# Kernel tuning notes

Hardware: AMD Instinct MI355X
Metric: run time of the kernel (lower is better)

Reference implementation:

```python
import jax, jax.numpy as jnp
import numpy as np

K = 8          # number of nearest neighbors (init kwarg k)
CONST = 0.1    # inverseweight const
NUM = 1.0      # inverseweight num


def setup_inputs() -> dict:
    key = jax.random.key(0)
    k1, k2 = jax.random.split(key)
    data1 = jax.random.normal(k1, (4096, 1024), dtype=jnp.float32)
    data2 = jax.random.normal(k2, (8192, 1024), dtype=jnp.float32)
    return {"data1": data1, "data2": data2}


def reference(data1, data2):
    # pairwise Euclidean distance (torch.dist with p=2): [N, M]
    x2 = jnp.sum(data1 * data1, axis=1, keepdims=True)          # [N, 1]
    y2 = jnp.sum(data2 * data2, axis=1)                         # [M]
    d2 = x2 + y2[None, :] - 2.0 * (data1 @ data2.T)             # [N, M]
    dist = jnp.sqrt(jnp.maximum(d2, 1e-12))

    # k smallest distances and their indices
    neg_top, idx = jax.lax.top_k(-dist, K)                      # [N, K]
    knn_dist = -neg_top                                         # [N, K]

    # inverse weighting: w = num / (dist + const)
    w = NUM / (knn_dist + CONST)                                # [N, K]

    # gather neighbor vectors and weighted-average them
    neigh = data2[idx]                                          # [N, K, D]
    out = jnp.einsum('nk,nkd->nd', w, neigh) / jnp.sum(w, axis=1, keepdims=True)
    return out
```

## Files before the change

### kernel.cpp

```cpp
#include <hip/hip_runtime.h>


typedef short bf16x8 __attribute__((ext_vector_type(8)));
typedef float f32x4 __attribute__((ext_vector_type(4)));

#define SENTINEL 1e30f
#define BKK 32

static __device__ __forceinline__ unsigned short f2bf(float f) {
  unsigned u = __float_as_uint(f);
  return (unsigned short)((u + 0x7fffu + ((u >> 16) & 1u)) >> 16);
}

__global__ __launch_bounds__(256) void convert_all_kernel(
    const float* __restrict__ A, const float* __restrict__ B,
    unsigned short* __restrict__ Abf, unsigned short* __restrict__ Bbf,
    float* __restrict__ y2, int N) {
  const int bid = blockIdx.x;
  const int tid = threadIdx.x;
  if (bid < N) {
    const float4 v = ((const float4*)&A[(size_t)bid * 1024])[tid];
    ushort4 o;
    o.x = f2bf(v.x); o.y = f2bf(v.y); o.z = f2bf(v.z); o.w = f2bf(v.w);
    ((ushort4*)&Abf[(size_t)bid * 1024])[tid] = o;
  } else {
    const int m = bid - N;
    __shared__ float red[256];
    const float4 v = ((const float4*)&B[(size_t)m * 1024])[tid];
    ushort4 o;
    o.x = f2bf(v.x); o.y = f2bf(v.y); o.z = f2bf(v.z); o.w = f2bf(v.w);
    ((ushort4*)&Bbf[(size_t)m * 1024])[tid] = o;
    red[tid] = v.x * v.x + v.y * v.y + v.z * v.z + v.w * v.w;
    __syncthreads();
    for (int s = 128; s > 0; s >>= 1) {
      if (tid < s) red[tid] += red[tid + s];
      __syncthreads();
    }
    if (tid == 0) y2[m] = red[0];
  }
}

#define CAS(sa, ia, sb, ib)                         \
  do {                                              \
    if ((sa) > (sb)) {                              \
      const float _t = (sa); (sa) = (sb); (sb) = _t;\
      const int _u = (ia); (ia) = (ib); (ib) = _u;  \
    }                                               \
  } while (0)

#define STAGE(sk, b)                                                          \
  do {                                                                        \
    const unsigned short* gA_ =                                               \
        Abf + (size_t)(r0 + w * 32 + srow) * 1024 + (sk) * 32 + sofs;         \
    const unsigned short* gB_ =                                               \
        Bbf + (size_t)(c0 + w * 64 + srow) * 1024 + (sk) * 32 + sofs;         \
    __builtin_amdgcn_global_load_lds(                                         \
        (const __attribute__((address_space(1))) void*)gA_,                   \
        (__attribute__((address_space(3))) void*)&As[b][(w * 32) * 32],       \
        16, 0, 0);                                                            \
    __builtin_amdgcn_global_load_lds(                                         \
        (const __attribute__((address_space(1))) void*)(gA_ + (size_t)16 * 1024), \
        (__attribute__((address_space(3))) void*)&As[b][(w * 32 + 16) * 32],  \
        16, 0, 0);                                                            \
    _Pragma("unroll")                                                         \
    for (int l_ = 0; l_ < 4; ++l_)                                            \
      __builtin_amdgcn_global_load_lds(                                       \
          (const __attribute__((address_space(1))) void*)(gB_ + (size_t)(16 * l_) * 1024), \
          (__attribute__((address_space(3))) void*)&Bs[b][(w * 64 + 16 * l_) * 32], \
          16, 0, 0);                                                          \
  } while (0)

#define COMPUTE(b)                                                            \
  do {                                                                        \
    bf16x8 af[4], bfr[8];                                                     \
    _Pragma("unroll")                                                         \
    for (int fi = 0; fi < 4; ++fi)                                            \
      af[fi] = *(const bf16x8*)&As[b][(frowA + fi * 16) * 32 + fofs];         \
    _Pragma("unroll")                                                         \
    for (int fj = 0; fj < 8; ++fj)                                            \
      bfr[fj] = *(const bf16x8*)&Bs[b][(frowB + fj * 16) * 32 + fofs];        \
    _Pragma("unroll")                                                         \
    for (int fi = 0; fi < 4; ++fi)                                            \
      _Pragma("unroll")                                                       \
      for (int fj = 0; fj < 8; ++fj)                                          \
        acc[fi][fj] = __builtin_amdgcn_mfma_f32_16x16x32_bf16(                \
            bfr[fj], af[fi], acc[fi][fj], 0, 0, 0);                           \
  } while (0)

__global__ __launch_bounds__(256, 2) void screen5_kernel(
    const unsigned short* __restrict__ Abf, const unsigned short* __restrict__ Bbf,
    const float* __restrict__ y2g,
    float* __restrict__ cand_s, int* __restrict__ cand_i) {
  __shared__ unsigned short As[2][128 * 32];
  __shared__ unsigned short Bs[2][256 * 32];
  __shared__ float y2sh[256];

  const int tid = threadIdx.x;
  const int w = tid >> 6;
  const int lane = tid & 63;
  const int wr = w >> 1, wc = w & 1;

  const int v = blockIdx.x + gridDim.x * blockIdx.y;
  const int bx = (v & 7) * 2 + ((v >> 3) & 1);
  const int by = v >> 4;
  const int r0 = by * 128;

  const int srow = lane >> 2;
  const int sofs = ((lane & 3) ^ ((lane >> 3) & 3)) * 8;

  const int frowA = wr * 64 + (lane & 15);
  const int frowB = wc * 128 + (lane & 15);
  const int fofs = ((lane >> 4) ^ ((lane >> 1) & 3)) * 8;
  const int cgrp = (lane >> 4) * 4;

  for (int chunk = 0; chunk < 2; ++chunk) {
    const int c0 = bx * 512 + chunk * 256;
    __syncthreads();
    y2sh[tid] = y2g[c0 + tid];

    f32x4 acc[4][8];
#pragma unroll
    for (int fi = 0; fi < 4; ++fi)
#pragma unroll
      for (int fj = 0; fj < 8; ++fj) {
        f32x4 z = {0.f, 0.f, 0.f, 0.f};
        acc[fi][fj] = z;
      }

    STAGE(0, 0);
    for (int kk = 0; kk < 32; kk += 2) {
      __syncthreads();
      STAGE(kk + 1, 1);
      COMPUTE(0);
      __syncthreads();
      if (kk + 2 < 32) STAGE(kk + 2, 0);
      COMPUTE(1);
    }

    float4 y2v[8];
#pragma unroll
    for (int fj = 0; fj < 8; ++fj)
      y2v[fj] = *(const float4*)&y2sh[wc * 128 + fj * 16 + cgrp];

#pragma unroll
    for (int fi = 0; fi < 4; ++fi) {
      float ls[8];
      int li[8];
#pragma unroll
      for (int j = 0; j < 8; ++j) { ls[j] = SENTINEL; li[j] = 0x7fffffff; }
      const int cb = c0 + wc * 128 + cgrp;
#pragma unroll
      for (int fj = 0; fj < 8; ++fj) {
#pragma unroll
        for (int reg = 0; reg < 4; ++reg) {
          const float s = y2v[fj][reg] - 2.0f * acc[fi][fj][reg];
          if (s < ls[7]) {
            ls[7] = s; li[7] = cb + fj * 16 + reg;
#pragma unroll
            for (int j = 7; j > 0; --j) {
              if (ls[j] < ls[j - 1]) {
                const float t = ls[j]; ls[j] = ls[j - 1]; ls[j - 1] = t;
                const int u = li[j]; li[j] = li[j - 1]; li[j - 1] = u;
              }
            }
          }
        }
      }
#pragma unroll
      for (int off = 16; off <= 32; off <<= 1) {
        float rs[8];
        int ri[8];
#pragma unroll
        for (int j = 0; j < 8; ++j) {
          rs[j] = __shfl_xor(ls[j], off, 64);
          ri[j] = __shfl_xor(li[j], off, 64);
        }
        float ms[8];
        int mi_[8];
#pragma unroll
        for (int i = 0; i < 8; ++i) {
          const bool t = ls[i] < rs[7 - i];
          ms[i] = t ? ls[i] : rs[7 - i];
          mi_[i] = t ? li[i] : ri[7 - i];
        }
        CAS(ms[0], mi_[0], ms[4], mi_[4]);
        CAS(ms[1], mi_[1], ms[5], mi_[5]);
        CAS(ms[2], mi_[2], ms[6], mi_[6]);
        CAS(ms[3], mi_[3], ms[7], mi_[7]);
        CAS(ms[0], mi_[0], ms[2], mi_[2]);
        CAS(ms[1], mi_[1], ms[3], mi_[3]);
        CAS(ms[4], mi_[4], ms[6], mi_[6]);
        CAS(ms[5], mi_[5], ms[7], mi_[7]);
        CAS(ms[0], mi_[0], ms[1], mi_[1]);
        CAS(ms[2], mi_[2], ms[3], mi_[3]);
        CAS(ms[4], mi_[4], ms[5], mi_[5]);
        CAS(ms[6], mi_[6], ms[7], mi_[7]);
#pragma unroll
        for (int j = 0; j < 8; ++j) { ls[j] = ms[j]; li[j] = mi_[j]; }
      }
      if ((lane >> 4) == 0) {
        const int row = r0 + wr * 64 + fi * 16 + lane;
        const size_t base =
            ((size_t)row * 64 + wc * 32 + bx * 2 + chunk) * 8;
#pragma unroll
        for (int j = 0; j < 8; ++j) {
          cand_s[base + j] = ls[j];
          cand_i[base + j] = li[j];
        }
      }
    }
  }
}

__global__ __launch_bounds__(256) void finalize4_kernel(
    const float* __restrict__ A, const float* __restrict__ B,
    const float* __restrict__ y2g,
    const float* __restrict__ cand_s, const int* __restrict__ cand_i,
    float* __restrict__ out) {
  const int tid = threadIdx.x;
  const int w = tid >> 6;
  const int lane = tid & 63;
  const int rloc = w >> 1;
  const int wh = w & 1;
  const int n = blockIdx.x * 2 + rloc;
  __shared__ int mi[2][512];
  __shared__ float comb[2][2][16];

  unsigned long long key[8];
#pragma unroll
  for (int i = 0; i < 8; ++i) {
    const int slot = lane + 64 * i;
    const float s = cand_s[(size_t)n * 512 + slot];
    if (wh == 0) mi[rloc][slot] = cand_i[(size_t)n * 512 + slot];
    unsigned u = __float_as_uint(s);
    u = (u & 0x80000000u) ? ~u : (u | 0x80000000u);
    key[i] = ((unsigned long long)u << 32) | (unsigned)slot;
  }
  __syncthreads();

  int ci[12];
  for (int r = 0; r < 12; ++r) {
    unsigned long long kb = key[0];
#pragma unroll
    for (int i = 1; i < 8; ++i) kb = key[i] < kb ? key[i] : kb;
#pragma unroll
    for (int off = 32; off >= 1; off >>= 1) {
      const unsigned long long o = __shfl_xor(kb, off, 64);
      kb = o < kb ? o : kb;
    }
    const int slot = (int)(kb & 0xffffffffu);
    ci[r] = mi[rloc][slot];
#pragma unroll
    for (int i = 0; i < 8; ++i)
      if (slot == lane + 64 * i) key[i] = ~0ull;
  }

  const float4* Arow = (const float4*)&A[(size_t)n * 1024];
  const int fbase = wh * 128 + lane * 2;
  float4 a4[2];
  a4[0] = Arow[fbase];
  a4[1] = Arow[fbase + 1];
  float part[13];
#pragma unroll
  for (int r = 0; r < 13; ++r) part[r] = 0.0f;
  part[12] = a4[0].x * a4[0].x + a4[0].y * a4[0].y + a4[0].z * a4[0].z +
             a4[0].w * a4[0].w + a4[1].x * a4[1].x + a4[1].y * a4[1].y +
             a4[1].z * a4[1].z + a4[1].w * a4[1].w;
#pragma unroll
  for (int p = 0; p < 2; ++p) {
    float4 b[12];
#pragma unroll
    for (int j = 0; j < 12; ++j)
      b[j] = ((const float4*)&B[(size_t)ci[j] * 1024])[fbase + p];
#pragma unroll
    for (int j = 0; j < 12; ++j)
      part[j] += a4[p].x * b[j].x + a4[p].y * b[j].y + a4[p].z * b[j].z +
                 a4[p].w * b[j].w;
  }
#pragma unroll
  for (int r = 0; r < 13; ++r) {
#pragma unroll
    for (int off = 32; off >= 1; off >>= 1) part[r] += __shfl_xor(part[r], off, 64);
  }
  if (lane == 0) {
#pragma unroll
    for (int r = 0; r < 13; ++r) comb[rloc][wh][r] = part[r];
  }
  __syncthreads();
  float tot[13];
#pragma unroll
  for (int r = 0; r < 13; ++r) tot[r] = comb[rloc][0][r] + comb[rloc][1][r];

  const float x2 = tot[12];
  float d2v[12];
  bool used[12];
#pragma unroll
  for (int j = 0; j < 12; ++j) {
    d2v[j] = x2 + y2g[ci[j]] - 2.0f * tot[j];
    used[j] = false;
  }
  float wk[8];
  int wi[8];
  float wsum = 0.0f;
  for (int k = 0; k < 8; ++k) {
    float bd = SENTINEL;
    int bi = 0x7fffffff, bslot = 0;
#pragma unroll
    for (int j = 0; j < 12; ++j) {
      if (used[j]) continue;
      const float d2 = d2v[j];
      if (d2 < bd || (d2 == bd && ci[j] < bi)) { bd = d2; bi = ci[j]; bslot = j; }
    }
    used[bslot] = true;
    const float d2c = fmaxf(bd, 1e-12f);
    const float wv = 1.0f / (sqrtf(d2c) + 0.1f);
    wk[k] = wv; wi[k] = bi; wsum += wv;
  }
  const float inv = 1.0f / wsum;

  float4 o0 = {0, 0, 0, 0}, o1 = {0, 0, 0, 0};
#pragma unroll
  for (int k = 0; k < 8; ++k) {
    const float wv = wk[k];
    const float4* Brow = (const float4*)&B[(size_t)wi[k] * 1024];
    const float4 b0 = Brow[fbase];
    const float4 b1 = Brow[fbase + 1];
    o0.x += wv * b0.x; o0.y += wv * b0.y; o0.z += wv * b0.z; o0.w += wv * b0.w;
    o1.x += wv * b1.x; o1.y += wv * b1.y; o1.z += wv * b1.z; o1.w += wv * b1.w;
  }
  o0.x *= inv; o0.y *= inv; o0.z *= inv; o0.w *= inv;
  o1.x *= inv; o1.y *= inv; o1.z *= inv; o1.w *= inv;
  float4* Orow = (float4*)&out[(size_t)n * 1024];
  Orow[fbase] = o0;
  Orow[fbase + 1] = o1;
}

__global__ __launch_bounds__(256) void rownorm_kernel(
    const float* __restrict__ B, float* __restrict__ y2) {
  const int m = blockIdx.x;
  const int tid = threadIdx.x;
  __shared__ float red[256];
  const float4 v = *(const float4*)&B[(size_t)m * 1024 + tid * 4];
  red[tid] = v.x * v.x + v.y * v.y + v.z * v.z + v.w * v.w;
  __syncthreads();
  for (int s = 128; s > 0; s >>= 1) {
    if (tid < s) red[tid] += red[tid + s];
    __syncthreads();
  }
  if (tid == 0) y2[m] = red[0];
}

__global__ __launch_bounds__(256) void knn_chunk_kernel(
    const float* __restrict__ A, const float* __restrict__ B,
    const float* __restrict__ y2g,
    float* __restrict__ cand_s, int* __restrict__ cand_i) {
  __shared__ float As[BKK][68];
  __shared__ float Bs[BKK][68];
  __shared__ float Sc[64][65];

  const int tid = threadIdx.x;
  const int tx = tid & 15;
  const int ty = tid >> 4;
  const int r0 = blockIdx.y * 64;
  const int c0 = blockIdx.x * 1024;
  const int lrow = tid >> 3;
  const int lk = (tid & 7) * 4;

  float top_s[8];
  int top_i[8];
#pragma unroll
  for (int j = 0; j < 8; ++j) { top_s[j] = SENTINEL; top_i[j] = 0x7fffffff; }

  for (int tile = 0; tile < 16; ++tile) {
    const int cbase = c0 + tile * 64;
    float acc[4][4];
#pragma unroll
    for (int i = 0; i < 4; ++i)
#pragma unroll
      for (int j = 0; j < 4; ++j) acc[i][j] = 0.0f;

    for (int k0 = 0; k0 < 1024; k0 += BKK) {
      const float4 a0 = *(const float4*)&A[(size_t)(r0 + lrow) * 1024 + k0 + lk];
      const float4 a1 = *(const float4*)&A[(size_t)(r0 + lrow + 32) * 1024 + k0 + lk];
      const float4 b0 = *(const float4*)&B[(size_t)(cbase + lrow) * 1024 + k0 + lk];
      const float4 b1 = *(const float4*)&B[(size_t)(cbase + lrow + 32) * 1024 + k0 + lk];
      __syncthreads();
      As[lk + 0][lrow] = a0.x; As[lk + 1][lrow] = a0.y;
      As[lk + 2][lrow] = a0.z; As[lk + 3][lrow] = a0.w;
      As[lk + 0][lrow + 32] = a1.x; As[lk + 1][lrow + 32] = a1.y;
      As[lk + 2][lrow + 32] = a1.z; As[lk + 3][lrow + 32] = a1.w;
      Bs[lk + 0][lrow] = b0.x; Bs[lk + 1][lrow] = b0.y;
      Bs[lk + 2][lrow] = b0.z; Bs[lk + 3][lrow] = b0.w;
      Bs[lk + 0][lrow + 32] = b1.x; Bs[lk + 1][lrow + 32] = b1.y;
      Bs[lk + 2][lrow + 32] = b1.z; Bs[lk + 3][lrow + 32] = b1.w;
      __syncthreads();
#pragma unroll
      for (int kk = 0; kk < BKK; ++kk) {
        const float4 av = *(const float4*)&As[kk][ty * 4];
        const float4 bv = *(const float4*)&Bs[kk][tx * 4];
        acc[0][0] += av.x * bv.x; acc[0][1] += av.x * bv.y;
        acc[0][2] += av.x * bv.z; acc[0][3] += av.x * bv.w;
        acc[1][0] += av.y * bv.x; acc[1][1] += av.y * bv.y;
        acc[1][2] += av.y * bv.z; acc[1][3] += av.y * bv.w;
        acc[2][0] += av.z * bv.x; acc[2][1] += av.z * bv.y;
        acc[2][2] += av.z * bv.z; acc[2][3] += av.z * bv.w;
        acc[3][0] += av.w * bv.x; acc[3][1] += av.w * bv.y;
        acc[3][2] += av.w * bv.z; acc[3][3] += av.w * bv.w;
      }
    }
#pragma unroll
    for (int i = 0; i < 4; ++i) {
      const int row = ty * 4 + i;
#pragma unroll
      for (int j = 0; j < 4; ++j) {
        const int col = tx * 4 + j;
        Sc[row][col] = y2g[cbase + col] - 2.0f * acc[i][j];
      }
    }
    __syncthreads();
    if (tid < 64) {
      for (int c = 0; c < 64; ++c) {
        const float s = Sc[tid][c];
        if (s < top_s[7]) {
          top_s[7] = s; top_i[7] = cbase + c;
#pragma unroll
          for (int j = 7; j > 0; --j) {
            if (top_s[j] < top_s[j - 1]) {
              const float tss = top_s[j]; top_s[j] = top_s[j - 1]; top_s[j - 1] = tss;
              const int tii = top_i[j]; top_i[j] = top_i[j - 1]; top_i[j - 1] = tii;
            }
          }
        }
      }
    }
  }

  if (tid < 64) {
    const int n = r0 + tid;
    const int base = (n * gridDim.x + blockIdx.x) * 8;
#pragma unroll
    for (int j = 0; j < 8; ++j) {
      cand_s[base + j] = top_s[j];
      cand_i[base + j] = top_i[j];
    }
  }
}

__global__ __launch_bounds__(256) void finalize_kernel(
    const float* __restrict__ A, const float* __restrict__ B,
    const float* __restrict__ cand_s, const int* __restrict__ cand_i,
    float* __restrict__ out, int nchunks) {
  const int n = blockIdx.x;
  const int tid = threadIdx.x;
  __shared__ float red[256];
  __shared__ float ls[64];
  __shared__ int li[64];
  __shared__ float wsh2[8];
  __shared__ int wid[8];
  __shared__ float wsum_sh;

  const int ncand = nchunks * 8;
  const float4 a = *(const float4*)&A[(size_t)n * 1024 + tid * 4];
  red[tid] = a.x * a.x + a.y * a.y + a.z * a.z + a.w * a.w;
  if (tid < ncand) {
    ls[tid] = cand_s[n * ncand + tid];
    li[tid] = cand_i[n * ncand + tid];
  }
  __syncthreads();
  for (int s = 128; s > 0; s >>= 1) {
    if (tid < s) red[tid] += red[tid + s];
    __syncthreads();
  }
  if (tid == 0) {
    const float x2 = red[0];
    float wsum = 0.0f;
    for (int j = 0; j < 8; ++j) {
      float bs = SENTINEL;
      int bi = 0x7fffffff;
      int bp = 0;
      for (int c = 0; c < ncand; ++c) {
        const float s_ = ls[c];
        const int i_ = li[c];
        if (s_ < bs || (s_ == bs && i_ < bi)) { bs = s_; bi = i_; bp = c; }
      }
      ls[bp] = SENTINEL; li[bp] = 0x7fffffff;
      float d2 = x2 + bs;
      d2 = fmaxf(d2, 1e-12f);
      const float wkk = 1.0f / (sqrtf(d2) + 0.1f);
      wsh2[j] = wkk; wid[j] = bi;
      wsum += wkk;
    }
    wsum_sh = wsum;
  }
  __syncthreads();
  const float inv = 1.0f / wsum_sh;
  float ox = 0.0f, oy = 0.0f, oz = 0.0f, ow = 0.0f;
#pragma unroll
  for (int j = 0; j < 8; ++j) {
    const float wkk = wsh2[j];
    const float4 v = *(const float4*)&B[(size_t)wid[j] * 1024 + tid * 4];
    ox += wkk * v.x; oy += wkk * v.y; oz += wkk * v.z; ow += wkk * v.w;
  }
  float4 o;
  o.x = ox * inv; o.y = oy * inv; o.z = oz * inv; o.w = ow * inv;
  *(float4*)&out[(size_t)n * 1024 + tid * 4] = o;
}

extern "C" void kernel_launch(void* const* d_in, const int* in_sizes, int n_in,
                              void* d_out, int out_size, void* d_ws, size_t ws_size,
                              hipStream_t stream) {
  const float* A = (const float*)d_in[0];
  const float* Bm = (const float*)d_in[1];
  const int D = 1024;
  const int N = in_sizes[0] / D;
  const int M = in_sizes[1] / D;

  const size_t needA = (size_t)N * D * 2;
  const size_t needB = (size_t)M * D * 2;
  const size_t needC = (size_t)N * 512 * 4;
  const size_t need = needA + needB + (size_t)M * 4 + 2 * needC;

  if (ws_size >= need && M == 8192 && N % 128 == 0 && N % 2 == 0) {
    unsigned short* Abf = (unsigned short*)d_ws;
    unsigned short* Bbf = Abf + (size_t)N * D;
    float* y2 = (float*)(Bbf + (size_t)M * D);
    float* cand_s = y2 + M;
    int* cand_i = (int*)(cand_s + (size_t)N * 512);

    convert_all_kernel<<<N + M, 256, 0, stream>>>(A, Bm, Abf, Bbf, y2, N);
    dim3 g(M / 512, N / 128);
    screen5_kernel<<<g, 256, 0, stream>>>(Abf, Bbf, y2, cand_s, cand_i);
    finalize4_kernel<<<N / 2, 256, 0, stream>>>(A, Bm, y2, cand_s, cand_i,
                                                (float*)d_out);
  } else {
    float* y2 = (float*)d_ws;
    float* cand_s = y2 + M;
    int* cand_i = (int*)(cand_s + (size_t)N * 64);
    rownorm_kernel<<<M, 256, 0, stream>>>(Bm, y2);
    dim3 gridB(M / 1024, N / 64);
    knn_chunk_kernel<<<gridB, 256, 0, stream>>>(A, Bm, y2, cand_s, cand_i);
    finalize_kernel<<<N, 256, 0, stream>>>(A, Bm, cand_s, cand_i, (float*)d_out, M / 1024);
  }
}
```

Measured before the change: 339.6 us.

## Triple-buffer GEMM staging with vmcnt sync and bitonic-merge finalize candidate selection

The screening GEMM moves from double to triple buffering of the LDS tiles. It uses explicit vmcnt waits with a single barrier per k-step and raises wave priority around the MFMA block, so global-to-LDS loads can run two stages ahead of compute. The y2 shared-memory staging is dropped in favour of direct global reads after the loop. The finalize kernel replaces its 12-round wave-wide argmin extraction with a register-level xor-shuffle bitonic merge of per-lane sorted top-8 lists into a top-12, which removes the LDS index table and the serial reductions. Triple buffering raises LDS use per block, which may reduce occupancy. Tie-breaking among equal scores may also differ from before.

```diff
diff --git a/kernel.cpp b/kernel.cpp
--- a/kernel.cpp
+++ b/kernel.cpp
@@ -79,21 +79,30 @@
     _Pragma("unroll")                                                         \
     for (int fj = 0; fj < 8; ++fj)                                            \
       bfr[fj] = *(const bf16x8*)&Bs[b][(frowB + fj * 16) * 32 + fofs];        \
+    __builtin_amdgcn_s_setprio(1);                                            \
     _Pragma("unroll")                                                         \
     for (int fi = 0; fi < 4; ++fi)                                            \
       _Pragma("unroll")                                                       \
       for (int fj = 0; fj < 8; ++fj)                                          \
         acc[fi][fj] = __builtin_amdgcn_mfma_f32_16x16x32_bf16(                \
             bfr[fj], af[fi], acc[fi][fj], 0, 0, 0);                           \
+    __builtin_amdgcn_s_setprio(0);                                            \
   } while (0)
 
-__global__ __launch_bounds__(256, 2) void screen5_kernel(
+#define PIPE_SYNC(N)                                                          \
+  do {                                                                        \
+    asm volatile("s_waitcnt vmcnt(" #N ")" ::: "memory");                     \
+    __builtin_amdgcn_sched_barrier(0);                                        \
+    __builtin_amdgcn_s_barrier();                                             \
+    __builtin_amdgcn_sched_barrier(0);                                        \
+  } while (0)
+
+__global__ __launch_bounds__(256, 2) void screen6_kernel(
     const unsigned short* __restrict__ Abf, const unsigned short* __restrict__ Bbf,
     const float* __restrict__ y2g,
     float* __restrict__ cand_s, int* __restrict__ cand_i) {
-  __shared__ unsigned short As[2][128 * 32];
-  __shared__ unsigned short Bs[2][256 * 32];
-  __shared__ float y2sh[256];
+  __shared__ unsigned short As[3][128 * 32];
+  __shared__ unsigned short Bs[3][256 * 32];
 
   const int tid = threadIdx.x;
   const int w = tid >> 6;
@@ -116,7 +125,6 @@
   for (int chunk = 0; chunk < 2; ++chunk) {
     const int c0 = bx * 512 + chunk * 256;
     __syncthreads();
-    y2sh[tid] = y2g[c0 + tid];
 
     f32x4 acc[4][8];
 #pragma unroll
@@ -128,19 +136,22 @@
       }
 
     STAGE(0, 0);
-    for (int kk = 0; kk < 32; kk += 2) {
-      __syncthreads();
-      STAGE(kk + 1, 1);
-      COMPUTE(0);
-      __syncthreads();
-      if (kk + 2 < 32) STAGE(kk + 2, 0);
-      COMPUTE(1);
-    }
+    STAGE(1, 1);
+    int cA = 0, cB = 1, cC = 2;
+    for (int t = 0; t < 31; ++t) {
+      PIPE_SYNC(6);
+      if (t < 30) STAGE(t + 2, cC);
+      __builtin_amdgcn_sched_barrier(0);
+      COMPUTE(cA);
+      const int tmp = cA; cA = cB; cB = cC; cC = tmp;
+    }
+    PIPE_SYNC(0);
+    COMPUTE(cA);
 
     float4 y2v[8];
 #pragma unroll
     for (int fj = 0; fj < 8; ++fj)
-      y2v[fj] = *(const float4*)&y2sh[wc * 128 + fj * 16 + cgrp];
+      y2v[fj] = *(const float4*)&y2g[c0 + wc * 128 + fj * 16 + cgrp];
 
 #pragma unroll
     for (int fi = 0; fi < 4; ++fi) {
@@ -212,7 +223,7 @@
   }
 }
 
-__global__ __launch_bounds__(256) void finalize4_kernel(
+__global__ __launch_bounds__(256) void finalize5_kernel(
     const float* __restrict__ A, const float* __restrict__ B,
     const float* __restrict__ y2g,
     const float* __restrict__ cand_s, const int* __restrict__ cand_i,
@@ -223,36 +234,52 @@
   const int rloc = w >> 1;
   const int wh = w & 1;
   const int n = blockIdx.x * 2 + rloc;
-  __shared__ int mi[2][512];
   __shared__ float comb[2][2][16];
 
-  unsigned long long key[8];
-#pragma unroll
-  for (int i = 0; i < 8; ++i) {
-    const int slot = lane + 64 * i;
-    const float s = cand_s[(size_t)n * 512 + slot];
-    if (wh == 0) mi[rloc][slot] = cand_i[(size_t)n * 512 + slot];
-    unsigned u = __float_as_uint(s);
-    u = (u & 0x80000000u) ? ~u : (u | 0x80000000u);
-    key[i] = ((unsigned long long)u << 32) | (unsigned)slot;
-  }
-  __syncthreads();
-
-  int ci[12];
-  for (int r = 0; r < 12; ++r) {
-    unsigned long long kb = key[0];
-#pragma unroll
-    for (int i = 1; i < 8; ++i) kb = key[i] < kb ? key[i] : kb;
-#pragma unroll
-    for (int off = 32; off >= 1; off >>= 1) {
-      const unsigned long long o = __shfl_xor(kb, off, 64);
-      kb = o < kb ? o : kb;
-    }
-    const int slot = (int)(kb & 0xffffffffu);
-    ci[r] = mi[rloc][slot];
-#pragma unroll
-    for (int i = 0; i < 8; ++i)
-      if (slot == lane + 64 * i) key[i] = ~0ull;
+  float s12[12];
+  int i12[12];
+  {
+    const float4* cs = (const float4*)&cand_s[(size_t)n * 512 + lane * 8];
+    const int4* cj = (const int4*)&cand_i[(size_t)n * 512 + lane * 8];
+    const float4 sa = cs[0], sb = cs[1];
+    const int4 ja = cj[0], jb = cj[1];
+    s12[0] = sa.x; s12[1] = sa.y; s12[2] = sa.z; s12[3] = sa.w;
+    s12[4] = sb.x; s12[5] = sb.y; s12[6] = sb.z; s12[7] = sb.w;
+    i12[0] = ja.x; i12[1] = ja.y; i12[2] = ja.z; i12[3] = ja.w;
+    i12[4] = jb.x; i12[5] = jb.y; i12[6] = jb.z; i12[7] = jb.w;
+#pragma unroll
+    for (int j = 8; j < 12; ++j) { s12[j] = SENTINEL; i12[j] = 0x7fffffff; }
+  }
+
+#pragma unroll
+  for (int off = 1; off <= 32; off <<= 1) {
+    float rs[12];
+    int ri[12];
+#pragma unroll
+    for (int j = 0; j < 12; ++j) {
+      rs[j] = __shfl_xor(s12[j], off, 64);
+      ri[j] = __shfl_xor(i12[j], off, 64);
+    }
+    float ms[12];
+    int mj[12];
+#pragma unroll
+    for (int j = 0; j < 12; ++j) {
+      const bool tke = s12[j] < rs[11 - j];
+      ms[j] = tke ? s12[j] : rs[11 - j];
+      mj[j] = tke ? i12[j] : ri[11 - j];
+    }
+    CAS(ms[0], mj[0], ms[8], mj[8]);  CAS(ms[1], mj[1], ms[9], mj[9]);
+    CAS(ms[2], mj[2], ms[10], mj[10]); CAS(ms[3], mj[3], ms[11], mj[11]);
+    CAS(ms[4], mj[4], ms[8], mj[8]);  CAS(ms[5], mj[5], ms[9], mj[9]);
+    CAS(ms[6], mj[6], ms[10], mj[10]); CAS(ms[7], mj[7], ms[11], mj[11]);
+    CAS(ms[0], mj[0], ms[2], mj[2]);  CAS(ms[1], mj[1], ms[3], mj[3]);
+    CAS(ms[4], mj[4], ms[6], mj[6]);  CAS(ms[5], mj[5], ms[7], mj[7]);
+    CAS(ms[8], mj[8], ms[10], mj[10]); CAS(ms[9], mj[9], ms[11], mj[11]);
+    CAS(ms[0], mj[0], ms[1], mj[1]);  CAS(ms[2], mj[2], ms[3], mj[3]);
+    CAS(ms[4], mj[4], ms[5], mj[5]);  CAS(ms[6], mj[6], ms[7], mj[7]);
+    CAS(ms[8], mj[8], ms[9], mj[9]);  CAS(ms[10], mj[10], ms[11], mj[11]);
+#pragma unroll
+    for (int j = 0; j < 12; ++j) { s12[j] = ms[j]; i12[j] = mj[j]; }
   }
 
   const float4* Arow = (const float4*)&A[(size_t)n * 1024];
@@ -271,7 +298,7 @@
     float4 b[12];
 #pragma unroll
     for (int j = 0; j < 12; ++j)
-      b[j] = ((const float4*)&B[(size_t)ci[j] * 1024])[fbase + p];
+      b[j] = ((const float4*)&B[(size_t)i12[j] * 1024])[fbase + p];
 #pragma unroll
     for (int j = 0; j < 12; ++j)
       part[j] += a4[p].x * b[j].x + a4[p].y * b[j].y + a4[p].z * b[j].z +
@@ -296,7 +323,7 @@
   bool used[12];
 #pragma unroll
   for (int j = 0; j < 12; ++j) {
-    d2v[j] = x2 + y2g[ci[j]] - 2.0f * tot[j];
+    d2v[j] = x2 + y2g[i12[j]] - 2.0f * tot[j];
     used[j] = false;
   }
   float wk[8];
@@ -309,7 +336,7 @@
     for (int j = 0; j < 12; ++j) {
       if (used[j]) continue;
       const float d2 = d2v[j];
-      if (d2 < bd || (d2 == bd && ci[j] < bi)) { bd = d2; bi = ci[j]; bslot = j; }
+      if (d2 < bd || (d2 == bd && i12[j] < bi)) { bd = d2; bi = i12[j]; bslot = j; }
     }
     used[bslot] = true;
     const float d2c = fmaxf(bd, 1e-12f);
@@ -529,8 +556,8 @@
 
     convert_all_kernel<<<N + M, 256, 0, stream>>>(A, Bm, Abf, Bbf, y2, N);
     dim3 g(M / 512, N / 128);
-    screen5_kernel<<<g, 256, 0, stream>>>(Abf, Bbf, y2, cand_s, cand_i);
-    finalize4_kernel<<<N / 2, 256, 0, stream>>>(A, Bm, y2, cand_s, cand_i,
+    screen6_kernel<<<g, 256, 0, stream>>>(Abf, Bbf, y2, cand_s, cand_i);
+    finalize5_kernel<<<N / 2, 256, 0, stream>>>(A, Bm, y2, cand_s, cand_i,
                                                 (float*)d_out);
   } else {
     float* y2 = (float*)d_ws;
```

Result: no change. 335.4 us (-1.2%).
